# Performance work log

Hardware: AMD Instinct MI355X
Metric: run time of the kernel (lower is better)

The kernel has to match this reference:

```python
import jax, jax.numpy as jnp
import numpy as np

B, L, D, H = 4, 1024, 1024, 16
HS = D // H
BLOCK = 1024
EPS = 1e-5


def setup_inputs() -> dict:
    key = jax.random.key(0)
    ks = jax.random.split(key, 12)
    s = 0.02
    return {
        "x": jax.random.normal(ks[0], (B, L, D), jnp.float32),
        "ln1_w": jnp.ones((D,), jnp.float32),
        "ln1_b": jnp.zeros((D,), jnp.float32),
        "Wqkv": jax.random.normal(ks[1], (D, 3 * D), jnp.float32) * s,
        "bqkv": jnp.zeros((3 * D,), jnp.float32),
        "Wproj": jax.random.normal(ks[2], (D, D), jnp.float32) * s,
        "bproj": jnp.zeros((D,), jnp.float32),
        "Er": jax.random.normal(ks[3], (BLOCK, HS), jnp.float32) * s,
        "ln2_w": jnp.ones((D,), jnp.float32),
        "ln2_b": jnp.zeros((D,), jnp.float32),
        "Wfc": jax.random.normal(ks[4], (D, 4 * D), jnp.float32) * s,
        "bfc": jnp.zeros((4 * D,), jnp.float32),
        "Wfc2": jax.random.normal(ks[5], (4 * D, D), jnp.float32) * s,
        "bfc2": jnp.zeros((D,), jnp.float32),
    }


def _layernorm(x, w, b):
    mu = jnp.mean(x, axis=-1, keepdims=True)
    var = jnp.mean(jnp.square(x - mu), axis=-1, keepdims=True)
    return (x - mu) * jax.lax.rsqrt(var + EPS) * w + b


def _skew(QEr):
    # Music-Transformer skew: pad one zero column on the left of last dim,
    # reshape (B,H,L,L+1) -> (B,H,L+1,L), drop first row.
    b, h, l, _ = QEr.shape
    padded = jnp.pad(QEr, ((0, 0), (0, 0), (0, 0), (1, 0)))
    return padded.reshape(b, h, l + 1, l)[:, :, 1:, :]


def _block(x, ln1_w, ln1_b, Wqkv, bqkv, Wproj, bproj, Er,
           ln2_w, ln2_b, Wfc, bfc, Wfc2, bfc2):
    b, l, d = x.shape
    # --- attention on ln_1(x) ---
    h = _layernorm(x, ln1_w, ln1_b)
    qkv = h @ Wqkv + bqkv                      # (B, L, 3D)
    q, k, v = jnp.split(qkv, 3, axis=-1)
    q = q.reshape(b, l, H, HS).transpose(0, 2, 1, 3)  # (B,H,L,hs)
    k = k.reshape(b, l, H, HS).transpose(0, 2, 1, 3)
    v = v.reshape(b, l, H, HS).transpose(0, 2, 1, 3)

    start = BLOCK - l
    Er_t = Er[start:, :].T                     # (hs, L)
    QEr = jnp.einsum('bhld,dm->bhlm', q, Er_t)  # (B,H,L,L)
    Srel = _skew(QEr)

    QKt = jnp.einsum('bhld,bhmd->bhlm', q, k)  # (B,H,L,L)
    scale = 1.0 / jnp.sqrt(jnp.asarray(HS, x.dtype))
    att = (QKt + Srel) * scale
    causal = jnp.tril(jnp.ones((l, l), bool))
    att = jnp.where(causal, att, jnp.asarray(-jnp.inf, att.dtype))
    att = jax.nn.softmax(att, axis=-1)
    y = jnp.einsum('bhlm,bhmd->bhld', att, v)  # (B,H,L,hs)
    y = y.transpose(0, 2, 1, 3).reshape(b, l, d)
    a = y @ Wproj + bproj

    x = x + a
    # --- MLP on ln_2(x) ---
    h2 = _layernorm(x, ln2_w, ln2_b)
    m = jax.nn.gelu(h2 @ Wfc + bfc, approximate=False) @ Wfc2 + bfc2
    return x + m


def reference(x, ln1_w, ln1_b, Wqkv, bqkv, Wproj, bproj, Er,
              ln2_w, ln2_b, Wfc, bfc, Wfc2, bfc2):
    return _block(x, ln1_w, ln1_b, Wqkv, bqkv, Wproj, bproj, Er,
                  ln2_w, ln2_b, Wfc, bfc, Wfc2, bfc2)
```

## Files before the change

### kernel.cpp

```cpp
#include <hip/hip_runtime.h>
#include <hip/hip_bf16.h>
#include <math.h>

typedef __attribute__((ext_vector_type(8))) __bf16 bf16x8;
typedef __attribute__((ext_vector_type(4))) float f32x4;

#define LL 1024
#define DD 1024
#define HH 16

#define GLOAD16(g, l)                                              \
  __builtin_amdgcn_global_load_lds(                                \
      (const __attribute__((address_space(1))) void*)(g),          \
      (__attribute__((address_space(3))) void*)(l), 16, 0, 0)

#define FENCE asm volatile("" ::: "memory")
#define BARRIER do { FENCE; __builtin_amdgcn_s_barrier(); FENCE; } while (0)
#define SCHEDB __builtin_amdgcn_sched_barrier(0)

__global__ __launch_bounds__(256) void transpose_cvt(const float* __restrict__ W,
                                                     __hip_bfloat16* __restrict__ Wt,
                                                     int R, int C) {
  __shared__ float tile[32][33];
  int tx = threadIdx.x;
  int r0 = blockIdx.y * 32, c0 = blockIdx.x * 32;
  int r = tx >> 3, c4 = (tx & 7) * 4;
  float4 v = *(const float4*)&W[(size_t)(r0 + r) * C + c0 + c4];
  tile[r][c4 + 0] = v.x; tile[r][c4 + 1] = v.y;
  tile[r][c4 + 2] = v.z; tile[r][c4 + 3] = v.w;
  __syncthreads();
  int c = tx >> 3, r4 = (tx & 7) * 4;
  __hip_bfloat16 o[4];
#pragma unroll
  for (int j = 0; j < 4; ++j) o[j] = __float2bfloat16(tile[r4 + j][c]);
  *(uint2*)&Wt[(size_t)(c0 + c) * R + r0 + r4] = *(const uint2*)o;
}

__global__ __launch_bounds__(256) void cvt_er(const float* __restrict__ Er,
                                              __hip_bfloat16* __restrict__ Erb) {
  int i = blockIdx.x * 256 + threadIdx.x;
  float4 v = *(const float4*)&Er[(size_t)i * 4];
  __hip_bfloat16 o[4];
  o[0] = __float2bfloat16(v.x); o[1] = __float2bfloat16(v.y);
  o[2] = __float2bfloat16(v.z); o[3] = __float2bfloat16(v.w);
  *(uint2*)&Erb[(size_t)i * 4] = *(const uint2*)o;
}

__global__ __launch_bounds__(256) void ln_kernel(const float* __restrict__ X,
                                                 const float* __restrict__ w,
                                                 const float* __restrict__ b,
                                                 __hip_bfloat16* __restrict__ out) {
  int row = blockIdx.x;
  int tid = threadIdx.x;
  const float* xr = X + (size_t)row * DD;
  float4 v = *(const float4*)&xr[tid * 4];
  float s = v.x + v.y + v.z + v.w;
  float s2 = v.x * v.x + v.y * v.y + v.z * v.z + v.w * v.w;
#pragma unroll
  for (int m = 1; m < 64; m <<= 1) {
    s += __shfl_xor(s, m);
    s2 += __shfl_xor(s2, m);
  }
  __shared__ float ps[4], ps2[4];
  int wv_ = tid >> 6, lane = tid & 63;
  if (lane == 0) { ps[wv_] = s; ps2[wv_] = s2; }
  __syncthreads();
  float ts = ps[0] + ps[1] + ps[2] + ps[3];
  float ts2 = ps2[0] + ps2[1] + ps2[2] + ps2[3];
  float mu = ts * (1.0f / DD);
  float var = ts2 * (1.0f / DD) - mu * mu;
  float rs = rsqrtf(var + 1e-5f);
  float4 wv = *(const float4*)&w[tid * 4];
  float4 bv = *(const float4*)&b[tid * 4];
  __hip_bfloat16 o[4];
  o[0] = __float2bfloat16((v.x - mu) * rs * wv.x + bv.x);
  o[1] = __float2bfloat16((v.y - mu) * rs * wv.y + bv.y);
  o[2] = __float2bfloat16((v.z - mu) * rs * wv.z + bv.z);
  o[3] = __float2bfloat16((v.w - mu) * rs * wv.w + bv.w);
  *(uint2*)&out[(size_t)row * DD + tid * 4] = *(const uint2*)o;
}

template <int EPI>
__global__ __launch_bounds__(512, 4) void gemm256x128(const __hip_bfloat16* __restrict__ A,
                                                      const __hip_bfloat16* __restrict__ Bt,
                                                      const float* __restrict__ bias,
                                                      const float* __restrict__ resid,
                                                      void* __restrict__ Cout,
                                                      int M, int N, int K) {
  __shared__ __hip_bfloat16 Ab[3][256][32];
  __shared__ __hip_bfloat16 Bb[3][128][32];
  const int tid = threadIdx.x, lane = tid & 63, w = tid >> 6;
  const int wm = w >> 1, wn = w & 1;

  int nbx = gridDim.x, nwg = nbx * gridDim.y;
  int orig = blockIdx.y * nbx + blockIdx.x;
  int cpx = nwg >> 3;
  int wgid = (orig & 7) * cpx + (orig >> 3);
  int bm0 = (wgid / nbx) * 256, bn0 = (wgid % nbx) * 128;

  const int fr = lane & 15, kq = lane >> 4;
  const int sg = ((lane & 3) ^ ((lane >> 3) & 3)) * 8;
  const int srw = lane >> 2;

  auto stageA = [&](int c, int g, int k0) {
    int u = w * 2 + g;
    const __hip_bfloat16* src = A + (size_t)(bm0 + u * 16 + srw) * K + k0 + sg;
    GLOAD16(src, (char*)Ab + c * 16384 + u * 1024);
  };
  auto stageB = [&](int c, int k0) {
    const __hip_bfloat16* src = Bt + (size_t)(bn0 + w * 16 + srw) * K + k0 + sg;
    GLOAD16(src, (char*)Bb + c * 8192 + w * 1024);
  };
  const int swz = ((kq ^ ((fr >> 1) & 3)) << 4);
  auto ldA = [&](int c, int r) -> bf16x8 {
    return *(const bf16x8*)((const char*)Ab + c * 16384 + r * 64 + swz);
  };
  auto ldB = [&](int c, int r) -> bf16x8 {
    return *(const bf16x8*)((const char*)Bb + c * 8192 + r * 64 + swz);
  };

  f32x4 acc[4][4] = {};
  bf16x8 a[4], b[4];

  const int nt = K >> 5;
#pragma unroll
  for (int tt = 0; tt < 2; ++tt) {
    stageA(tt, 0, tt * 32); stageA(tt, 1, tt * 32); stageB(tt, tt * 32);
  }
  asm volatile("s_waitcnt vmcnt(3)" ::: "memory");
  BARRIER;

  int cur = 0, nxt = 2;
  for (int t = 0; t < nt; ++t) {
#pragma unroll
    for (int mf = 0; mf < 4; ++mf) a[mf] = ldA(cur, wm * 64 + mf * 16 + fr);
#pragma unroll
    for (int nf = 0; nf < 4; ++nf) b[nf] = ldB(cur, wn * 64 + nf * 16 + fr);
    if (t + 2 < nt) {
      stageA(nxt, 0, (t + 2) * 32); stageA(nxt, 1, (t + 2) * 32); stageB(nxt, (t + 2) * 32);
    }
    __builtin_amdgcn_s_setprio(1);
#pragma unroll
    for (int mf = 0; mf < 4; ++mf)
#pragma unroll
      for (int nf = 0; nf < 4; ++nf)
        acc[mf][nf] = __builtin_amdgcn_mfma_f32_16x16x32_bf16(a[mf], b[nf], acc[mf][nf], 0, 0, 0);
    __builtin_amdgcn_s_setprio(0);
    if (t <= nt - 3)      { asm volatile("s_waitcnt vmcnt(3)" ::: "memory"); }
    else if (t == nt - 2) { asm volatile("s_waitcnt vmcnt(0)" ::: "memory"); }
    BARRIER;
    cur = (cur == 2) ? 0 : cur + 1;
    nxt = (nxt == 2) ? 0 : nxt + 1;
  }

#pragma unroll
  for (int nf = 0; nf < 4; ++nf) {
    int col = bn0 + wn * 64 + nf * 16 + fr;
    float bsv = bias[col];
#pragma unroll
    for (int mf = 0; mf < 4; ++mf) {
      int rowb = bm0 + wm * 64 + mf * 16 + kq * 4;
#pragma unroll
      for (int j = 0; j < 4; ++j) {
        int row = rowb + j;
        float v = acc[mf][nf][j] + bsv;
        if (EPI == 1) v = 0.5f * v * (1.0f + erff(v * 0.7071067811865476f));
        if (EPI == 2) {
          ((float*)Cout)[(size_t)row * N + col] = v + resid[(size_t)row * N + col];
        } else {
          ((__hip_bfloat16*)Cout)[(size_t)row * N + col] = __float2bfloat16(v);
        }
      }
    }
  }
}

template <int EPI>
__global__ __launch_bounds__(256, 2) void gemm128x64(const __hip_bfloat16* __restrict__ A,
                                                     const __hip_bfloat16* __restrict__ Bt,
                                                     const float* __restrict__ bias,
                                                     const float* __restrict__ resid,
                                                     void* __restrict__ Cout,
                                                     int M, int N, int K) {
  __shared__ __hip_bfloat16 Ab[3][128][32];
  __shared__ __hip_bfloat16 Bb[3][64][32];
  const int tid = threadIdx.x, lane = tid & 63, w = tid >> 6;
  const int wm = w >> 1, wn = w & 1;

  int nbx = gridDim.x, nwg = nbx * gridDim.y;
  int orig = blockIdx.y * nbx + blockIdx.x;
  int cpx = nwg >> 3;
  int wgid = (orig & 7) * cpx + (orig >> 3);
  int bm0 = (wgid / nbx) * 128, bn0 = (wgid % nbx) * 64;

  const int fr = lane & 15, kq = lane >> 4;
  const int sg = ((lane & 3) ^ ((lane >> 3) & 3)) * 8;
  const int srw = lane >> 2;

  auto stageA = [&](int c, int g, int k0) {
    int u = w * 2 + g;
    const __hip_bfloat16* src = A + (size_t)(bm0 + u * 16 + srw) * K + k0 + sg;
    GLOAD16(src, (char*)Ab + c * 8192 + u * 1024);
  };
  auto stageB = [&](int c, int k0) {
    const __hip_bfloat16* src = Bt + (size_t)(bn0 + w * 16 + srw) * K + k0 + sg;
    GLOAD16(src, (char*)Bb + c * 4096 + w * 1024);
  };
  const int swz = ((kq ^ ((fr >> 1) & 3)) << 4);
  auto ldA = [&](int c, int r) -> bf16x8 {
    return *(const bf16x8*)((const char*)Ab + c * 8192 + r * 64 + swz);
  };
  auto ldB = [&](int c, int r) -> bf16x8 {
    return *(const bf16x8*)((const char*)Bb + c * 4096 + r * 64 + swz);
  };

  f32x4 acc[4][2] = {};
  bf16x8 a[4], b[2];

  const int nt = K >> 5;
#pragma unroll
  for (int tt = 0; tt < 2; ++tt) {
    stageA(tt, 0, tt * 32); stageA(tt, 1, tt * 32); stageB(tt, tt * 32);
  }
  asm volatile("s_waitcnt vmcnt(3)" ::: "memory");
  BARRIER;

  int cur = 0, nxt = 2;
  for (int t = 0; t < nt; ++t) {
#pragma unroll
    for (int mf = 0; mf < 4; ++mf) a[mf] = ldA(cur, wm * 64 + mf * 16 + fr);
#pragma unroll
    for (int nf = 0; nf < 2; ++nf) b[nf] = ldB(cur, wn * 32 + nf * 16 + fr);
    if (t + 2 < nt) {
      stageA(nxt, 0, (t + 2) * 32); stageA(nxt, 1, (t + 2) * 32); stageB(nxt, (t + 2) * 32);
    }
    __builtin_amdgcn_s_setprio(1);
#pragma unroll
    for (int mf = 0; mf < 4; ++mf)
#pragma unroll
      for (int nf = 0; nf < 2; ++nf)
        acc[mf][nf] = __builtin_amdgcn_mfma_f32_16x16x32_bf16(a[mf], b[nf], acc[mf][nf], 0, 0, 0);
    __builtin_amdgcn_s_setprio(0);
    if (t <= nt - 3)      { asm volatile("s_waitcnt vmcnt(3)" ::: "memory"); }
    else if (t == nt - 2) { asm volatile("s_waitcnt vmcnt(0)" ::: "memory"); }
    BARRIER;
    cur = (cur == 2) ? 0 : cur + 1;
    nxt = (nxt == 2) ? 0 : nxt + 1;
  }

#pragma unroll
  for (int nf = 0; nf < 2; ++nf) {
    int col = bn0 + wn * 32 + nf * 16 + fr;
    float bsv = bias[col];
#pragma unroll
    for (int mf = 0; mf < 4; ++mf) {
      int rowb = bm0 + wm * 64 + mf * 16 + kq * 4;
#pragma unroll
      for (int j = 0; j < 4; ++j) {
        int row = rowb + j;
        float v = acc[mf][nf][j] + bsv;
        if (EPI == 1) v = 0.5f * v * (1.0f + erff(v * 0.7071067811865476f));
        if (EPI == 2) {
          ((float*)Cout)[(size_t)row * N + col] = v + resid[(size_t)row * N + col];
        } else {
          ((__hip_bfloat16*)Cout)[(size_t)row * N + col] = __float2bfloat16(v);
        }
      }
    }
  }
}

__global__ __launch_bounds__(256) void attn_mfma(const __hip_bfloat16* __restrict__ qkv,
                                                 const __hip_bfloat16* __restrict__ Erb,
                                                 __hip_bfloat16* __restrict__ Y) {
  __shared__ __hip_bfloat16 k_s[64][72];
  __shared__ __hip_bfloat16 er_s[128][72];
  __shared__ __hip_bfloat16 p_s[4][16][72];
  __shared__ __hip_bfloat16 g_s[4][16][132];
  __shared__ __hip_bfloat16 vt_s[64 * 64];

  int bid = blockIdx.x;
  int qi = 15 - (bid >> 6);
  int head = bid & 63;
  int h = head & 15, b = head >> 4;
  int l0 = qi * 64;
  int tid = threadIdx.x, lane = tid & 63, w = tid >> 6;
  const int fr = lane & 15, kq = lane >> 4;

  const __hip_bfloat16* base = qkv + (size_t)b * (LL * 3072) + h * 64;

  bf16x8 qf[2];
  {
    const __hip_bfloat16* q0 = base + (size_t)(l0 + 16 * w + fr) * 3072 + kq * 8;
    qf[0] = *(const bf16x8*)q0;
    qf[1] = *(const bf16x8*)(q0 + 32);
  }

  const int ksr = tid >> 2, ksd = (tid & 3) * 16;
  const __hip_bfloat16* ksrc = base + 1024 + (size_t)ksr * 3072 + ksd;
  const int vc = (tid >> 3) * 2, vd0 = (tid & 7) * 8;
  const __hip_bfloat16* vsrc = base + 2048 + (size_t)vc * 3072 + vd0;
  const int e0r = tid >> 1, e0c = (tid & 1) * 32;
  const int err = tid >> 2, erc = (tid & 3) * 16;

  uint4 kst0, kst1, vst0, vst1;
  uint4 est0, est1, est2, est3;
  uint4 ers0, ers1;

  {
    kst0 = *(const uint4*)ksrc; kst1 = *(const uint4*)(ksrc + 8);
    vst0 = *(const uint4*)vsrc; vst1 = *(const uint4*)(vsrc + 3072);
    int m = min(max(960 - l0 + e0r, 0), 1023);
    const __hip_bfloat16* ep = Erb + (size_t)m * 64 + e0c;
    est0 = *(const uint4*)ep;        est1 = *(const uint4*)(ep + 8);
    est2 = *(const uint4*)(ep + 16); est3 = *(const uint4*)(ep + 24);
  }

  f32x4 oacc[4] = {};
  float m_run[4], s_run[4];
#pragma unroll
  for (int j = 0; j < 4; ++j) { m_run[j] = -1e30f; s_run[j] = 0.f; }

  auto gchunk = [&](int hf) {
#pragma unroll
    for (int g = 0; g < 4; ++g) {
      int cc = hf * 64 + 16 * g + fr, kc = kq * 8;
      bf16x8 e0 = *(const bf16x8*)&er_s[cc][kc];
      bf16x8 e1 = *(const bf16x8*)&er_s[cc][kc + 32];
      f32x4 gacc = {};
      gacc = __builtin_amdgcn_mfma_f32_16x16x32_bf16(qf[0], e0, gacc, 0, 0, 0);
      gacc = __builtin_amdgcn_mfma_f32_16x16x32_bf16(qf[1], e1, gacc, 0, 0, 0);
#pragma unroll
      for (int j = 0; j < 4; ++j)
        g_s[w][kq * 4 + j][hf * 64 + 16 * g + fr] = __float2bfloat16(gacc[j]);
    }
  };

  for (int t = 0; t <= qi; ++t) {
    __syncthreads();
    *(uint4*)&k_s[ksr][ksd] = kst0;
    *(uint4*)&k_s[ksr][ksd + 8] = kst1;
    {
      const uint16_t* h0 = (const uint16_t*)&vst0;
      const uint16_t* h1 = (const uint16_t*)&vst1;
#pragma unroll
      for (int j = 0; j < 8; ++j) {
        int d = vd0 + j;
        uint32_t pk = (uint32_t)h0[j] | ((uint32_t)h1[j] << 16);
        uint32_t byte = ((uint32_t)d << 7) + 2u * (uint32_t)vc;
        byte ^= (uint32_t)(((d & 7) ^ (d >> 3)) << 4);
        *(uint32_t*)((char*)vt_s + byte) = pk;
      }
    }
    if (t == 0) {
      *(uint4*)&er_s[e0r][e0c]      = est0;
      *(uint4*)&er_s[e0r][e0c + 8]  = est1;
      *(uint4*)&er_s[e0r][e0c + 16] = est2;
      *(uint4*)&er_s[e0r][e0c + 24] = est3;
    } else if (t < qi) {
      int hf = (t + 1) & 1;
      *(uint4*)&er_s[hf * 64 + err][erc]     = ers0;
      *(uint4*)&er_s[hf * 64 + err][erc + 8] = ers1;
    }
    __syncthreads();
    if (t < qi) {
      int c0n = (t + 1) * 64;
      const __hip_bfloat16* kp = ksrc + (size_t)c0n * 3072;
      kst0 = *(const uint4*)kp; kst1 = *(const uint4*)(kp + 8);
      const __hip_bfloat16* vp = vsrc + (size_t)c0n * 3072;
      vst0 = *(const uint4*)vp; vst1 = *(const uint4*)(vp + 3072);
      if (t + 1 < qi) {
        int m = min(960 - l0 + (t + 2) * 64 + err, 1023);
        const __hip_bfloat16* ep = Erb + (size_t)m * 64 + erc;
        ers0 = *(const uint4*)ep; ers1 = *(const uint4*)(ep + 8);
      }
    }
    SCHEDB;

    f32x4 sacc[4] = {};
#pragma unroll
    for (int f = 0; f < 4; ++f) {
      int cc = 16 * f + fr, kc = kq * 8;
      bf16x8 k0 = *(const bf16x8*)&k_s[cc][kc];
      bf16x8 k1 = *(const bf16x8*)&k_s[cc][kc + 32];
      sacc[f] = __builtin_amdgcn_mfma_f32_16x16x32_bf16(qf[0], k0, sacc[f], 0, 0, 0);
      sacc[f] = __builtin_amdgcn_mfma_f32_16x16x32_bf16(qf[1], k1, sacc[f], 0, 0, 0);
    }
    if (t == 0) {
      gchunk(0);
      if (qi > 0) gchunk(1);
    } else if (t < qi) {
      gchunk((t + 1) & 1);
    }

    float sv[4][4];
#pragma unroll
    for (int f = 0; f < 4; ++f) {
#pragma unroll
      for (int j = 0; j < 4; ++j) {
        int r = kq * 4 + j;
        int c = 16 * f + fr;
        int jj = c - (16 * w + r) + 63;
        float g = __bfloat162float(g_s[w][r][(t * 64 + jj) & 127]);
        float val = (sacc[f][j] + g) * 0.125f;
        if (t == qi && c > 16 * w + r) val = -1e30f;
        sv[f][j] = val;
      }
    }
    float alpha[4];
#pragma unroll
    for (int j = 0; j < 4; ++j) {
      float tm = fmaxf(fmaxf(sv[0][j], sv[1][j]), fmaxf(sv[2][j], sv[3][j]));
      tm = fmaxf(tm, __shfl_xor(tm, 1));
      tm = fmaxf(tm, __shfl_xor(tm, 2));
      tm = fmaxf(tm, __shfl_xor(tm, 4));
      tm = fmaxf(tm, __shfl_xor(tm, 8));
      float nm = fmaxf(m_run[j], tm);
      alpha[j] = __expf(m_run[j] - nm);
      m_run[j] = nm;
    }
#pragma unroll
    for (int f = 0; f < 4; ++f)
#pragma unroll
      for (int j = 0; j < 4; ++j)
        sv[f][j] = __expf(sv[f][j] - m_run[j]);
#pragma unroll
    for (int j = 0; j < 4; ++j) {
      float ps = sv[0][j] + sv[1][j] + sv[2][j] + sv[3][j];
      ps += __shfl_xor(ps, 1); ps += __shfl_xor(ps, 2);
      ps += __shfl_xor(ps, 4); ps += __shfl_xor(ps, 8);
      s_run[j] = s_run[j] * alpha[j] + ps;
    }
#pragma unroll
    for (int f = 0; f < 4; ++f)
#pragma unroll
      for (int j = 0; j < 4; ++j)
        oacc[f][j] *= alpha[j];
#pragma unroll
    for (int f = 0; f < 4; ++f)
#pragma unroll
      for (int j = 0; j < 4; ++j)
        p_s[w][kq * 4 + j][16 * f + fr] = __float2bfloat16(sv[f][j]);
#pragma unroll
    for (int kk = 0; kk < 2; ++kk) {
      bf16x8 pf = *(const bf16x8*)&p_s[w][fr][kq * 8 + 32 * kk];
#pragma unroll
      for (int f = 0; f < 4; ++f) {
        int d = 16 * f + fr;
        int cc = kq * 8 + 32 * kk;
        uint32_t byte = ((uint32_t)d << 7) + 2u * (uint32_t)cc;
        byte ^= (uint32_t)(((d & 7) ^ (d >> 3)) << 4);
        bf16x8 vf = *(const bf16x8*)((char*)vt_s + byte);
        oacc[f] = __builtin_amdgcn_mfma_f32_16x16x32_bf16(pf, vf, oacc[f], 0, 0, 0);
      }
    }
  }

#pragma unroll
  for (int f = 0; f < 4; ++f)
#pragma unroll
    for (int j = 0; j < 4; ++j) {
      int r = 16 * w + kq * 4 + j;
      int d = 16 * f + fr;
      float o = oacc[f][j] / s_run[j];
      Y[(size_t)(b * LL + l0 + r) * DD + h * 64 + d] = __float2bfloat16(o);
    }
}

extern "C" void kernel_launch(void* const* d_in, const int* in_sizes, int n_in,
                              void* d_out, int out_size, void* d_ws, size_t ws_size,
                              hipStream_t stream) {
  (void)in_sizes; (void)n_in; (void)out_size; (void)ws_size;
  const float* x     = (const float*)d_in[0];
  const float* ln1w  = (const float*)d_in[1];
  const float* ln1b  = (const float*)d_in[2];
  const float* Wqkv  = (const float*)d_in[3];
  const float* bqkv  = (const float*)d_in[4];
  const float* Wproj = (const float*)d_in[5];
  const float* bproj = (const float*)d_in[6];
  const float* Er    = (const float*)d_in[7];
  const float* ln2w  = (const float*)d_in[8];
  const float* ln2b  = (const float*)d_in[9];
  const float* Wfc   = (const float*)d_in[10];
  const float* bfc   = (const float*)d_in[11];
  const float* Wfc2  = (const float*)d_in[12];
  const float* bfc2  = (const float*)d_in[13];
  float* out = (float*)d_out;

  char* ws = (char*)d_ws;
  const size_t MB = 1ull << 20;
  __hip_bfloat16* h1    = (__hip_bfloat16*)(ws + 0);
  __hip_bfloat16* qkvb  = (__hip_bfloat16*)(ws + 8 * MB);
  __hip_bfloat16* mbuf  = (__hip_bfloat16*)(ws + 0);
  __hip_bfloat16* yb    = (__hip_bfloat16*)(ws + 32 * MB);
  __hip_bfloat16* h2    = (__hip_bfloat16*)(ws + 32 * MB);
  float*          x2    = (float*)(ws + 40 * MB);
  __hip_bfloat16* Wqkvt = (__hip_bfloat16*)(ws + 56 * MB);
  __hip_bfloat16* Erb   = (__hip_bfloat16*)(ws + 62 * MB);
  __hip_bfloat16* Wprojt= (__hip_bfloat16*)(ws + 63 * MB);
  __hip_bfloat16* Wfct  = (__hip_bfloat16*)(ws + 66 * MB);
  __hip_bfloat16* Wfc2t = (__hip_bfloat16*)(ws + 75 * MB);

  dim3 blk(256);

  transpose_cvt<<<dim3(3072 / 32, 1024 / 32), blk, 0, stream>>>(Wqkv, Wqkvt, 1024, 3072);
  transpose_cvt<<<dim3(1024 / 32, 1024 / 32), blk, 0, stream>>>(Wproj, Wprojt, 1024, 1024);
  transpose_cvt<<<dim3(4096 / 32, 1024 / 32), blk, 0, stream>>>(Wfc, Wfct, 1024, 4096);
  transpose_cvt<<<dim3(1024 / 32, 4096 / 32), blk, 0, stream>>>(Wfc2, Wfc2t, 4096, 1024);
  cvt_er<<<dim3(64), blk, 0, stream>>>(Er, Erb);

  ln_kernel<<<4096, blk, 0, stream>>>(x, ln1w, ln1b, h1);

  gemm256x128<0><<<dim3(3072 / 128, 4096 / 256), dim3(512), 0, stream>>>(
      h1, Wqkvt, bqkv, nullptr, qkvb, 4096, 3072, 1024);

  attn_mfma<<<dim3(1024), blk, 0, stream>>>(qkvb, Erb, yb);

  gemm128x64<2><<<dim3(1024 / 64, 4096 / 128), blk, 0, stream>>>(
      yb, Wprojt, bproj, x, x2, 4096, 1024, 1024);

  ln_kernel<<<4096, blk, 0, stream>>>(x2, ln2w, ln2b, h2);

  gemm256x128<1><<<dim3(4096 / 128, 4096 / 256), dim3(512), 0, stream>>>(
      h2, Wfct, bfc, nullptr, mbuf, 4096, 4096, 1024);

  gemm128x64<2><<<dim3(1024 / 64, 4096 / 128), blk, 0, stream>>>(
      mbuf, Wfc2t, bfc2, x2, out, 4096, 1024, 4096);
}
```

Baseline: 251.7 us.

## Use 8-wave 128x64 GEMM with K=64 stages and shrink attention Er buffer

The projection and FC2 GEMMs move from 4 waves to 8 waves per block, each wave covering a 32x32 sub-tile. The K step per stage doubles to 64 with a new XOR swizzle, and the launch bounds target 4 blocks per CU. Separately, the attention kernel's Er shared buffer is halved to 64 rows by staging the second initial chunk through registers, at the cost of two extra barriers on the first iteration. The goal is more waves in flight and lower LDS use, which risks higher per-block LDS in the GEMM and extra synchronization.

```diff
diff --git a/kernel.cpp b/kernel.cpp
--- a/kernel.cpp
+++ b/kernel.cpp
@@ -176,14 +176,14 @@
 }
 
 template <int EPI>
-__global__ __launch_bounds__(256, 2) void gemm128x64(const __hip_bfloat16* __restrict__ A,
-                                                     const __hip_bfloat16* __restrict__ Bt,
-                                                     const float* __restrict__ bias,
-                                                     const float* __restrict__ resid,
-                                                     void* __restrict__ Cout,
-                                                     int M, int N, int K) {
-  __shared__ __hip_bfloat16 Ab[3][128][32];
-  __shared__ __hip_bfloat16 Bb[3][64][32];
+__global__ __launch_bounds__(512, 4) void gemm128x64w8(const __hip_bfloat16* __restrict__ A,
+                                                       const __hip_bfloat16* __restrict__ Bt,
+                                                       const float* __restrict__ bias,
+                                                       const float* __restrict__ resid,
+                                                       void* __restrict__ Cout,
+                                                       int M, int N, int K) {
+  __shared__ __hip_bfloat16 Ab[3][128][64];
+  __shared__ __hip_bfloat16 Bb[3][64][64];
   const int tid = threadIdx.x, lane = tid & 63, w = tid >> 6;
   const int wm = w >> 1, wn = w & 1;
 
@@ -194,33 +194,34 @@
   int bm0 = (wgid / nbx) * 128, bn0 = (wgid % nbx) * 64;
 
   const int fr = lane & 15, kq = lane >> 4;
-  const int sg = ((lane & 3) ^ ((lane >> 3) & 3)) * 8;
-  const int srw = lane >> 2;
-
-  auto stageA = [&](int c, int g, int k0) {
-    int u = w * 2 + g;
-    const __hip_bfloat16* src = A + (size_t)(bm0 + u * 16 + srw) * K + k0 + sg;
-    GLOAD16(src, (char*)Ab + c * 8192 + u * 1024);
+  const int srw = lane >> 3;
+  const int sg = ((lane & 7) ^ (lane >> 3)) * 8;
+
+  auto stageA = [&](int c, int j, int k0) {
+    int u = 2 * w + j;
+    const __hip_bfloat16* src = A + (size_t)(bm0 + u * 8 + srw) * K + k0 + sg;
+    GLOAD16(src, (char*)Ab + c * 16384 + u * 1024);
   };
   auto stageB = [&](int c, int k0) {
-    const __hip_bfloat16* src = Bt + (size_t)(bn0 + w * 16 + srw) * K + k0 + sg;
-    GLOAD16(src, (char*)Bb + c * 4096 + w * 1024);
-  };
-  const int swz = ((kq ^ ((fr >> 1) & 3)) << 4);
-  auto ldA = [&](int c, int r) -> bf16x8 {
-    return *(const bf16x8*)((const char*)Ab + c * 8192 + r * 64 + swz);
-  };
-  auto ldB = [&](int c, int r) -> bf16x8 {
-    return *(const bf16x8*)((const char*)Bb + c * 4096 + r * 64 + swz);
-  };
-
-  f32x4 acc[4][2] = {};
-  bf16x8 a[4], b[2];
-
-  const int nt = K >> 5;
+    const __hip_bfloat16* src = Bt + (size_t)(bn0 + w * 8 + srw) * K + k0 + sg;
+    GLOAD16(src, (char*)Bb + c * 8192 + w * 1024);
+  };
+  auto ldA = [&](int c, int r, int ks) -> bf16x8 {
+    int byte = r * 128 + ((ks * 64 + kq * 16) ^ ((r & 7) << 4));
+    return *(const bf16x8*)((const char*)Ab + c * 16384 + byte);
+  };
+  auto ldB = [&](int c, int r, int ks) -> bf16x8 {
+    int byte = r * 128 + ((ks * 64 + kq * 16) ^ ((r & 7) << 4));
+    return *(const bf16x8*)((const char*)Bb + c * 8192 + byte);
+  };
+
+  f32x4 acc[2][2] = {};
+  bf16x8 a[2][2], b[2][2];
+
+  const int nt = K >> 6;
 #pragma unroll
   for (int tt = 0; tt < 2; ++tt) {
-    stageA(tt, 0, tt * 32); stageA(tt, 1, tt * 32); stageB(tt, tt * 32);
+    stageA(tt, 0, tt * 64); stageA(tt, 1, tt * 64); stageB(tt, tt * 64);
   }
   asm volatile("s_waitcnt vmcnt(3)" ::: "memory");
   BARRIER;
@@ -228,18 +229,27 @@
   int cur = 0, nxt = 2;
   for (int t = 0; t < nt; ++t) {
 #pragma unroll
-    for (int mf = 0; mf < 4; ++mf) a[mf] = ldA(cur, wm * 64 + mf * 16 + fr);
-#pragma unroll
-    for (int nf = 0; nf < 2; ++nf) b[nf] = ldB(cur, wn * 32 + nf * 16 + fr);
+    for (int mf = 0; mf < 2; ++mf)
+#pragma unroll
+      for (int ks = 0; ks < 2; ++ks)
+        a[mf][ks] = ldA(cur, wm * 32 + mf * 16 + fr, ks);
+#pragma unroll
+    for (int nf = 0; nf < 2; ++nf)
+#pragma unroll
+      for (int ks = 0; ks < 2; ++ks)
+        b[nf][ks] = ldB(cur, wn * 32 + nf * 16 + fr, ks);
     if (t + 2 < nt) {
-      stageA(nxt, 0, (t + 2) * 32); stageA(nxt, 1, (t + 2) * 32); stageB(nxt, (t + 2) * 32);
+      stageA(nxt, 0, (t + 2) * 64); stageA(nxt, 1, (t + 2) * 64); stageB(nxt, (t + 2) * 64);
     }
     __builtin_amdgcn_s_setprio(1);
 #pragma unroll
-    for (int mf = 0; mf < 4; ++mf)
+    for (int mf = 0; mf < 2; ++mf)
 #pragma unroll
       for (int nf = 0; nf < 2; ++nf)
-        acc[mf][nf] = __builtin_amdgcn_mfma_f32_16x16x32_bf16(a[mf], b[nf], acc[mf][nf], 0, 0, 0);
+#pragma unroll
+        for (int ks = 0; ks < 2; ++ks)
+          acc[mf][nf] = __builtin_amdgcn_mfma_f32_16x16x32_bf16(
+              a[mf][ks], b[nf][ks], acc[mf][nf], 0, 0, 0);
     __builtin_amdgcn_s_setprio(0);
     if (t <= nt - 3)      { asm volatile("s_waitcnt vmcnt(3)" ::: "memory"); }
     else if (t == nt - 2) { asm volatile("s_waitcnt vmcnt(0)" ::: "memory"); }
@@ -253,8 +263,8 @@
     int col = bn0 + wn * 32 + nf * 16 + fr;
     float bsv = bias[col];
 #pragma unroll
-    for (int mf = 0; mf < 4; ++mf) {
-      int rowb = bm0 + wm * 64 + mf * 16 + kq * 4;
+    for (int mf = 0; mf < 2; ++mf) {
+      int rowb = bm0 + wm * 32 + mf * 16 + kq * 4;
 #pragma unroll
       for (int j = 0; j < 4; ++j) {
         int row = rowb + j;
@@ -274,7 +284,7 @@
                                                  const __hip_bfloat16* __restrict__ Erb,
                                                  __hip_bfloat16* __restrict__ Y) {
   __shared__ __hip_bfloat16 k_s[64][72];
-  __shared__ __hip_bfloat16 er_s[128][72];
+  __shared__ __hip_bfloat16 er_s[64][72];
   __shared__ __hip_bfloat16 p_s[4][16][72];
   __shared__ __hip_bfloat16 g_s[4][16][132];
   __shared__ __hip_bfloat16 vt_s[64 * 64];
@@ -300,20 +310,23 @@
   const __hip_bfloat16* ksrc = base + 1024 + (size_t)ksr * 3072 + ksd;
   const int vc = (tid >> 3) * 2, vd0 = (tid & 7) * 8;
   const __hip_bfloat16* vsrc = base + 2048 + (size_t)vc * 3072 + vd0;
-  const int e0r = tid >> 1, e0c = (tid & 1) * 32;
   const int err = tid >> 2, erc = (tid & 3) * 16;
 
   uint4 kst0, kst1, vst0, vst1;
-  uint4 est0, est1, est2, est3;
   uint4 ers0, ers1;
+  uint4 ec10, ec11;
 
   {
     kst0 = *(const uint4*)ksrc; kst1 = *(const uint4*)(ksrc + 8);
     vst0 = *(const uint4*)vsrc; vst1 = *(const uint4*)(vsrc + 3072);
-    int m = min(max(960 - l0 + e0r, 0), 1023);
-    const __hip_bfloat16* ep = Erb + (size_t)m * 64 + e0c;
-    est0 = *(const uint4*)ep;        est1 = *(const uint4*)(ep + 8);
-    est2 = *(const uint4*)(ep + 16); est3 = *(const uint4*)(ep + 24);
+    int m0 = min(max(960 - l0 + err, 0), 1023);
+    const __hip_bfloat16* ep0 = Erb + (size_t)m0 * 64 + erc;
+    ers0 = *(const uint4*)ep0; ers1 = *(const uint4*)(ep0 + 8);
+    if (qi > 0) {
+      int m1 = min(max(960 - l0 + 64 + err, 0), 1023);
+      const __hip_bfloat16* ep1 = Erb + (size_t)m1 * 64 + erc;
+      ec10 = *(const uint4*)ep1; ec11 = *(const uint4*)(ep1 + 8);
+    }
   }
 
   f32x4 oacc[4] = {};
@@ -324,7 +337,7 @@
   auto gchunk = [&](int hf) {
 #pragma unroll
     for (int g = 0; g < 4; ++g) {
-      int cc = hf * 64 + 16 * g + fr, kc = kq * 8;
+      int cc = 16 * g + fr, kc = kq * 8;
       bf16x8 e0 = *(const bf16x8*)&er_s[cc][kc];
       bf16x8 e1 = *(const bf16x8*)&er_s[cc][kc + 32];
       f32x4 gacc = {};
@@ -352,15 +365,9 @@
         *(uint32_t*)((char*)vt_s + byte) = pk;
       }
     }
-    if (t == 0) {
-      *(uint4*)&er_s[e0r][e0c]      = est0;
-      *(uint4*)&er_s[e0r][e0c + 8]  = est1;
-      *(uint4*)&er_s[e0r][e0c + 16] = est2;
-      *(uint4*)&er_s[e0r][e0c + 24] = est3;
-    } else if (t < qi) {
-      int hf = (t + 1) & 1;
-      *(uint4*)&er_s[hf * 64 + err][erc]     = ers0;
-      *(uint4*)&er_s[hf * 64 + err][erc + 8] = ers1;
+    if (t == 0 || t < qi) {
+      *(uint4*)&er_s[err][erc]     = ers0;
+      *(uint4*)&er_s[err][erc + 8] = ers1;
     }
     __syncthreads();
     if (t < qi) {
@@ -388,7 +395,13 @@
     }
     if (t == 0) {
       gchunk(0);
-      if (qi > 0) gchunk(1);
+      if (qi > 0) {
+        __syncthreads();
+        *(uint4*)&er_s[err][erc]     = ec10;
+        *(uint4*)&er_s[err][erc + 8] = ec11;
+        __syncthreads();
+        gchunk(1);
+      }
     } else if (t < qi) {
       gchunk((t + 1) & 1);
     }
@@ -516,7 +529,7 @@
 
   attn_mfma<<<dim3(1024), blk, 0, stream>>>(qkvb, Erb, yb);
 
-  gemm128x64<2><<<dim3(1024 / 64, 4096 / 128), blk, 0, stream>>>(
+  gemm128x64w8<2><<<dim3(1024 / 64, 4096 / 128), dim3(512), 0, stream>>>(
       yb, Wprojt, bproj, x, x2, 4096, 1024, 1024);
 
   ln_kernel<<<4096, blk, 0, stream>>>(x2, ln2w, ln2b, h2);
@@ -524,6 +537,6 @@
   gemm256x128<1><<<dim3(4096 / 128, 4096 / 256), dim3(512), 0, stream>>>(
       h2, Wfct, bfc, nullptr, mbuf, 4096, 4096, 1024);
 
-  gemm128x64<2><<<dim3(1024 / 64, 4096 / 128), blk, 0, stream>>>(
+  gemm128x64w8<2><<<dim3(1024 / 64, 4096 / 128), dim3(512), 0, stream>>>(
       mbuf, Wfc2t, bfc2, x2, out, 4096, 1024, 4096);
 }
```

After: 226.0 us. -10.2%, faster.
